# Performance work log

Hardware: AMD Instinct MI355X
Metric: run time of the kernel (lower is better)

The kernel has to match this reference:

```python
import jax, jax.numpy as jnp
import numpy as np

B, T, C, H, N, FF = 2, 1024, 2048, 32, 64, 8192
DIV = 8.0  # head_size_divisor
LAYER_ID, N_LAYER = 1, 24
EPS = 1e-5


def _layer_norm(x, g, b):
    m = x.mean(-1, keepdims=True)
    v = x.var(-1, keepdims=True)
    return (x - m) / jnp.sqrt(v + EPS) * g + b


def _group_norm(x, g, b):
    # GroupNorm(H, C) applied per token: normalize each head's N channels
    xg = x.reshape(B, T, H, N)
    m = xg.mean(-1, keepdims=True)
    v = xg.var(-1, keepdims=True)
    xn = ((xg - m) / jnp.sqrt(v + EPS)).reshape(B, T, C)
    return xn * g + b


def _time_shift(x):
    # xx[t] = x[t-1], xx[0] = 0
    return jnp.pad(x, ((0, 0), (1, 0), (0, 0)))[:, :-1]


def _wkv5(r, k, v, w, u):
    # r,k,v: [B,T,H,N]; w,u: [H,N]. Linear recurrence with per-channel decay.
    decay = jnp.exp(-jnp.exp(w))            # [H,N]
    dec = decay[None, :, :, None]           # broadcast over B and v-dim
    uu = u[None, :, :, None]
    rs = jnp.moveaxis(r, 1, 0)              # [T,B,H,N]
    ks = jnp.moveaxis(k, 1, 0)
    vs = jnp.moveaxis(v, 1, 0)

    def step(state, inp):                   # state: [B,H,N,N] (k-dim i, v-dim j)
        rt, kt, vt = inp
        kv = kt[..., :, None] * vt[..., None, :]          # [B,H,N,N]
        y = jnp.einsum('bhi,bhij->bhj', rt, uu * kv + state)
        return dec * state + kv, y

    state0 = jnp.zeros((B, H, N, N), r.dtype)
    _, ys = jax.lax.scan(step, state0, (rs, ks, vs))
    return jnp.moveaxis(ys, 0, 1).reshape(B, T, C)


def _forward(x, ln1_g, ln1_b, ln2_g, ln2_b,
             tm_k, tm_v, tm_r, tm_g, time_decay, time_faaaa,
             Wr, Wk, Wv, Wg, Wo, lnx_g, lnx_b,
             fm_k, fm_r, Wkey, Wrec, Wval):
    # ---- TimeMix ----
    xl = _layer_norm(x, ln1_g, ln1_b)
    xx = _time_shift(xl)
    xk = xl * tm_k + xx * (1 - tm_k)
    xv = xl * tm_v + xx * (1 - tm_v)
    xr = xl * tm_r + xx * (1 - tm_r)
    xg = xl * tm_g + xx * (1 - tm_g)
    r = (xr @ Wr).reshape(B, T, H, N)
    k = (xk @ Wk).reshape(B, T, H, N)
    v = (xv @ Wv).reshape(B, T, H, N)
    g = jax.nn.silu(xg @ Wg)
    att = _wkv5(r, k, v, time_decay, time_faaaa)
    att = _group_norm(att / DIV, lnx_g, lnx_b)
    x = x + (att * g) @ Wo
    # ---- ChannelMix ----
    xl2 = _layer_norm(x, ln2_g, ln2_b)
    xx2 = _time_shift(xl2)
    ck = xl2 * fm_k + xx2 * (1 - fm_k)
    cr = xl2 * fm_r + xx2 * (1 - fm_r)
    kk = jnp.square(jax.nn.relu(ck @ Wkey))
    kv = kk @ Wval
    return x + jax.nn.sigmoid(cr @ Wrec) * kv


def setup_inputs() -> dict:
    key = jax.random.key(0)
    ks = jax.random.split(key, 9)
    r01 = LAYER_ID / (N_LAYER - 1)
    r1a0 = 1.0 - LAYER_ID / N_LAYER
    ddd = (np.arange(C, dtype=np.float64) / C)[None, None, :]
    dec = np.array([-6 + 5 * (n / (C - 1)) ** (0.7 + 1.3 * r01) for n in range(C)])
    faa = np.array([r01 * (1 - n / (C - 1)) + ((n + 1) % 3 - 1) * 0.1 for n in range(C)])
    f32 = lambda a: jnp.asarray(a, jnp.float32)
    w = lambda k_, i, o: jax.random.normal(k_, (i, o), jnp.float32) * (i ** -0.5)
    return {
        'x': jax.random.normal(ks[0], (B, T, C), jnp.float32),
        'ln1_g': jnp.ones((C,), jnp.float32), 'ln1_b': jnp.zeros((C,), jnp.float32),
        'ln2_g': jnp.ones((C,), jnp.float32), 'ln2_b': jnp.zeros((C,), jnp.float32),
        'tm_k': f32(ddd ** r1a0), 'tm_v': f32(ddd ** r1a0 + 0.3 * r01),
        'tm_r': f32(ddd ** (0.5 * r1a0)), 'tm_g': f32(ddd ** (0.5 * r1a0)),
        'time_decay': f32(dec.reshape(H, N)), 'time_faaaa': f32(faa.reshape(H, N)),
        'Wr': w(ks[1], C, C), 'Wk': w(ks[2], C, C), 'Wv': w(ks[3], C, C),
        'Wg': w(ks[4], C, C), 'Wo': w(ks[5], C, C),
        'lnx_g': jnp.ones((C,), jnp.float32), 'lnx_b': jnp.zeros((C,), jnp.float32),
        'fm_k': f32(ddd ** r1a0), 'fm_r': f32(ddd ** r1a0),
        'Wkey': w(ks[6], C, FF), 'Wrec': w(ks[7], C, C), 'Wval': w(ks[8], FF, C),
    }


def reference(x, ln1_g, ln1_b, ln2_g, ln2_b,
              tm_k, tm_v, tm_r, tm_g, time_decay, time_faaaa,
              Wr, Wk, Wv, Wg, Wo, lnx_g, lnx_b,
              fm_k, fm_r, Wkey, Wrec, Wval):
    return _forward(x, ln1_g, ln1_b, ln2_g, ln2_b,
                    tm_k, tm_v, tm_r, tm_g, time_decay, time_faaaa,
                    Wr, Wk, Wv, Wg, Wo, lnx_g, lnx_b,
                    fm_k, fm_r, Wkey, Wrec, Wval)
```

## Files before the change

kernel.cpp:

```cpp
#include <hip/hip_runtime.h>
#include <stdint.h>

#define BB 2
#define TT 1024
#define CC 2048
#define HH 32
#define NNH 64
#define FFD 8192
#define MTOT (BB*TT)
#define LNEPS 1e-5f
#define LOG2E 1.44269504088896340736f

typedef __attribute__((ext_vector_type(8))) __bf16 bf16x8;
typedef __attribute__((ext_vector_type(4))) float f32x4;

#define USE_GLL 1
typedef __attribute__((address_space(1))) void GAS;
typedef __attribute__((address_space(3))) void LAS;

__device__ inline void gload_lds16(const uint16_t* g, uint16_t* l) {
#if USE_GLL
  __builtin_amdgcn_global_load_lds((GAS*)g, (LAS*)l, 16, 0, 0);
#else
  *(uint4*)l = *(const uint4*)g;
#endif
}

__device__ inline float bf2f(uint32_t u) {
  union { uint32_t i; float f; } v; v.i = u << 16; return v.f;
}
__device__ inline uint16_t f2bf(float f) {
  union { float f; uint32_t i; } v; v.f = f;
  uint32_t r = v.i + 0x7FFFu + ((v.i >> 16) & 1u);
  return (uint16_t)(r >> 16);
}
__device__ inline void unpack8(uint4 d, float* v) {
  v[0] = bf2f(d.x & 0xffffu); v[1] = bf2f(d.x >> 16);
  v[2] = bf2f(d.y & 0xffffu); v[3] = bf2f(d.y >> 16);
  v[4] = bf2f(d.z & 0xffffu); v[5] = bf2f(d.z >> 16);
  v[6] = bf2f(d.w & 0xffffu); v[7] = bf2f(d.w >> 16);
}
__device__ inline uint4 pack8(const float* v) {
  uint4 d;
  d.x = (uint32_t)f2bf(v[0]) | ((uint32_t)f2bf(v[1]) << 16);
  d.y = (uint32_t)f2bf(v[2]) | ((uint32_t)f2bf(v[3]) << 16);
  d.z = (uint32_t)f2bf(v[4]) | ((uint32_t)f2bf(v[5]) << 16);
  d.w = (uint32_t)f2bf(v[6]) | ((uint32_t)f2bf(v[7]) << 16);
  return d;
}

__device__ inline void load8f(const void* p, size_t idx, int fl, float* v) {
  if (fl) {
    const float* q = (const float*)p + idx;
    float4 a = *(const float4*)q; float4 b = *(const float4*)(q + 4);
    v[0]=a.x; v[1]=a.y; v[2]=a.z; v[3]=a.w; v[4]=b.x; v[5]=b.y; v[6]=b.z; v[7]=b.w;
  } else {
    unpack8(*(const uint4*)((const uint16_t*)p + idx), v);
  }
}
__device__ inline float load1f(const void* p, size_t idx, int fl) {
  return fl ? ((const float*)p)[idx] : bf2f(((const uint16_t*)p)[idx]);
}

__global__ void probe_kernel(const uint16_t* __restrict__ x, int* __restrict__ flag) {
  int tid = threadIdx.x;
  float m = 0.f;
  for (int i = tid; i < 4096; i += 64) {
    float a = fabsf(bf2f(x[i]));
    if (a > m) m = a;
  }
  for (int o = 32; o; o >>= 1) { float t = __shfl_down(m, o); if (t > m) m = t; }
  if (tid == 0) *flag = (m > 1e6f) ? 1 : 0;
}

template<int INMODE>
__global__ __launch_bounds__(256) void ln_kernel(const void* __restrict__ x,
    const void* __restrict__ g, const void* __restrict__ b,
    uint16_t* __restrict__ out, const int* __restrict__ dflag)
{
  int fl = *dflag;
  int row = blockIdx.x;
  int tid = threadIdx.x;
  int lane = tid & 63, wave = tid >> 6;
  size_t base = (size_t)row * CC + (size_t)tid * 8;
  float v[8];
  if constexpr (INMODE == 1) {
    const float* q = (const float*)x + base;
    float4 a = *(const float4*)q; float4 c = *(const float4*)(q + 4);
    v[0]=a.x; v[1]=a.y; v[2]=a.z; v[3]=a.w; v[4]=c.x; v[5]=c.y; v[6]=c.z; v[7]=c.w;
  } else {
    load8f(x, base, fl, v);
  }
  float s = 0.f, s2 = 0.f;
  #pragma unroll
  for (int j = 0; j < 8; j++) { s += v[j]; s2 += v[j] * v[j]; }
  for (int o = 32; o; o >>= 1) { s += __shfl_down(s, o); s2 += __shfl_down(s2, o); }
  __shared__ float red[8];
  if (lane == 0) { red[wave] = s; red[wave + 4] = s2; }
  __syncthreads();
  s  = red[0] + red[1] + red[2] + red[3];
  s2 = red[4] + red[5] + red[6] + red[7];
  float mean = s * (1.0f / CC);
  float var  = s2 * (1.0f / CC) - mean * mean;
  float rstd = rsqrtf(fmaxf(var, 0.f) + LNEPS);
  float gj[8], bj[8];
  load8f(g, (size_t)tid * 8, fl, gj);
  load8f(b, (size_t)tid * 8, fl, bj);
  float o8[8];
  #pragma unroll
  for (int j = 0; j < 8; j++) o8[j] = (v[j] - mean) * rstd * gj[j] + bj[j];
  *(uint4*)(out + base) = pack8(o8);
}

__global__ __launch_bounds__(256) void mix4_kernel(const uint16_t* __restrict__ xl,
    const void* __restrict__ tmr, const void* __restrict__ tmk,
    const void* __restrict__ tmv, const void* __restrict__ tmg,
    uint16_t* __restrict__ out, const int* __restrict__ dflag)
{
  int fl = *dflag;
  uint32_t idx = ((uint32_t)blockIdx.x * 256u + threadIdx.x) * 8u;
  uint32_t c = idx & (CC - 1);
  uint32_t row = idx >> 11;
  uint32_t t = row & (TT - 1);
  float xv[8], pv[8];
  unpack8(*(const uint4*)(xl + idx), xv);
  if (t) { unpack8(*(const uint4*)(xl + idx - CC), pv); }
  else   { for (int j = 0; j < 8; j++) pv[j] = 0.f; }
  const void* tms[4] = { tmr, tmk, tmv, tmg };
  const size_t SL = (size_t)MTOT * CC;
  #pragma unroll
  for (int a = 0; a < 4; a++) {
    float tm[8], o[8];
    load8f(tms[a], c, fl, tm);
    #pragma unroll
    for (int j = 0; j < 8; j++) o[j] = xv[j] * tm[j] + pv[j] * (1.f - tm[j]);
    *(uint4*)(out + a * SL + idx) = pack8(o);
  }
}

__global__ __launch_bounds__(256) void mix2_kernel(const uint16_t* __restrict__ xl,
    const void* __restrict__ tk, const void* __restrict__ tr,
    uint16_t* __restrict__ ok, uint16_t* __restrict__ orr,
    const int* __restrict__ dflag)
{
  int fl = *dflag;
  uint32_t idx = ((uint32_t)blockIdx.x * 256u + threadIdx.x) * 8u;
  uint32_t c = idx & (CC - 1);
  uint32_t row = idx >> 11;
  uint32_t t = row & (TT - 1);
  float xv[8], pv[8], tm[8], o[8];
  unpack8(*(const uint4*)(xl + idx), xv);
  if (t) { unpack8(*(const uint4*)(xl + idx - CC), pv); }
  else   { for (int j = 0; j < 8; j++) pv[j] = 0.f; }
  load8f(tk, c, fl, tm);
  #pragma unroll
  for (int j = 0; j < 8; j++) o[j] = xv[j] * tm[j] + pv[j] * (1.f - tm[j]);
  *(uint4*)(ok + idx) = pack8(o);
  load8f(tr, c, fl, tm);
  #pragma unroll
  for (int j = 0; j < 8; j++) o[j] = xv[j] * tm[j] + pv[j] * (1.f - tm[j]);
  *(uint4*)(orr + idx) = pack8(o);
}

__device__ inline void transpose_tile(const void* W, uint16_t* WT, int Kd, int Nd,
                                      int n0, int k0, int fl, int tid)
{
  __shared__ __align__(16) uint16_t tile[64][66];
  int r = tid >> 3, s = tid & 7;
  #pragma unroll
  for (int p = 0; p < 2; p++) {
    int row = p * 32 + r;
    float tv[8];
    load8f(W, (size_t)(k0 + row) * Nd + n0 + s * 8, fl, tv);
    uint16_t* t = &tile[row][s * 8];
    #pragma unroll
    for (int e = 0; e < 8; e++) t[e] = f2bf(tv[e]);
  }
  __syncthreads();
  #pragma unroll
  for (int p = 0; p < 2; p++) {
    int row = p * 32 + r;
    uint16_t tmp[8];
    #pragma unroll
    for (int e = 0; e < 8; e++) tmp[e] = tile[s * 8 + e][row];
    uint4 o;
    o.x = (uint32_t)tmp[0] | ((uint32_t)tmp[1] << 16);
    o.y = (uint32_t)tmp[2] | ((uint32_t)tmp[3] << 16);
    o.z = (uint32_t)tmp[4] | ((uint32_t)tmp[5] << 16);
    o.w = (uint32_t)tmp[6] | ((uint32_t)tmp[7] << 16);
    *(uint4*)(WT + (size_t)(n0 + row) * Kd + k0 + s * 8) = o;
  }
}

__global__ __launch_bounds__(256) void transpose_kernel(const void* __restrict__ W,
    uint16_t* __restrict__ WT, int Kd, int Nd, const int* __restrict__ dflag)
{
  transpose_tile(W, WT, Kd, Nd, blockIdx.x * 64, blockIdx.y * 64, *dflag, threadIdx.x);
}

__global__ __launch_bounds__(256) void transpose4_kernel(
    const void* __restrict__ W0, const void* __restrict__ W1,
    const void* __restrict__ W2, const void* __restrict__ W3,
    uint16_t* __restrict__ WT, const int* __restrict__ dflag)
{
  const void* Ws[4] = { W0, W1, W2, W3 };
  int z = blockIdx.z;
  transpose_tile(Ws[z], WT + (size_t)z * CC * CC, CC, CC,
                 blockIdx.x * 64, blockIdx.y * 64, *dflag, threadIdx.x);
}

enum { EPI_RESID = 2, EPI_SIGM = 9 };

template<int EPI>
__global__ __launch_bounds__(256, 2) void gemm_kernel(
    const uint16_t* __restrict__ Ain, const uint16_t* __restrict__ BTin,
    void* __restrict__ Cout, int N, int Kstride, int Kloop,
    const void* __restrict__ auxA, const int* __restrict__ dflag)
{
  const uint16_t* A  = Ain;
  const uint16_t* BT = BTin;
  uint16_t* co16 = (uint16_t*)Cout;
  float*    co32 = (float*)Cout;
  int fl = 0;
  if constexpr (EPI == EPI_RESID) fl = *dflag;
  int bx = blockIdx.x;
  int N_ = N;
  int n0 = bx * 128;
  int m0 = blockIdx.y * 128;
  __shared__ __align__(16) uint16_t As[128 * 64];
  __shared__ __align__(16) uint16_t Bs[128 * 64];
  int tid = threadIdx.x;
  int lane = tid & 63, wave = tid >> 6;
  int wm = (wave >> 1) * 64, wn = (wave & 1) * 64;
  int l15 = lane & 15, lq = lane >> 4;
  int sw = l15 & 7;
  f32x4 acc[4][4];
  #pragma unroll
  for (int i = 0; i < 4; i++)
    #pragma unroll
    for (int j = 0; j < 4; j++) acc[i][j] = 0.f;
  const int rr = tid >> 3, seg = tid & 7;
  const int sseg = (seg ^ (rr & 7)) * 8;
  const uint16_t* Ag = A + (size_t)(m0 + rr) * Kstride + sseg;
  const uint16_t* Bg = BT + (size_t)(n0 + rr) * Kstride + sseg;
  uint16_t* Asw = As + tid * 8;
  uint16_t* Bsw = Bs + tid * 8;
  for (int k0 = 0; k0 < Kloop; k0 += 64) {
    __syncthreads();
    #pragma unroll
    for (int p = 0; p < 4; p++) {
      gload_lds16(Ag + (size_t)p * 32 * Kstride + k0, Asw + p * 2048);
      gload_lds16(Bg + (size_t)p * 32 * Kstride + k0, Bsw + p * 2048);
    }
    __syncthreads();
    #pragma unroll
    for (int kk = 0; kk < 2; kk++) {
      int cidx = ((kk * 4 + lq) ^ sw) * 8;
      bf16x8 af[4], bv[4];
      #pragma unroll
      for (int f = 0; f < 4; f++) af[f] = *(const bf16x8*)&As[(wm + f * 16 + l15) * 64 + cidx];
      #pragma unroll
      for (int f = 0; f < 4; f++) bv[f] = *(const bf16x8*)&Bs[(wn + f * 16 + l15) * 64 + cidx];
      #pragma unroll
      for (int fm = 0; fm < 4; fm++)
        #pragma unroll
        for (int fn = 0; fn < 4; fn++)
          acc[fm][fn] = __builtin_amdgcn_mfma_f32_16x16x32_bf16(af[fm], bv[fn], acc[fm][fn], 0, 0, 0);
    }
  }
  #pragma unroll
  for (int fm = 0; fm < 4; fm++) {
    #pragma unroll
    for (int q = 0; q < 4; q++) {
      int gr = m0 + wm + fm * 16 + lq * 4 + q;
      size_t rowb = (size_t)gr * N_;
      #pragma unroll
      for (int fn = 0; fn < 4; fn++) {
        int gc = n0 + wn + fn * 16 + l15;
        size_t idx = rowb + gc;
        float val = acc[fm][fn][q];
        if constexpr (EPI == EPI_RESID) {
          co32[idx] = val + load1f(auxA, idx, fl);
        } else if constexpr (EPI == EPI_SIGM) {
          co16[idx] = f2bf(1.f / (1.f + __expf(-val)));
        }
      }
    }
  }
}

enum { G_RKVG = 0, G_KK = 1, G_PART = 2 };

template<int EPI>
__global__ __launch_bounds__(512, 2) void gemm256_kernel(
    const uint16_t* __restrict__ Ain, const uint16_t* __restrict__ BTin,
    void* __restrict__ Cout, int N, int Kstride, int Kloop, int cx,
    float* __restrict__ p2, float* __restrict__ p3a, float* __restrict__ p3b)
{
  __shared__ __align__(16) uint16_t smem[65536];
  const uint16_t* A  = Ain;
  const uint16_t* BT = BTin;
  uint16_t* co16 = (uint16_t*)Cout;
  float*    co32 = (float*)Cout;

  uint32_t lid = ((uint32_t)blockIdx.z * gridDim.y + blockIdx.y) * gridDim.x + blockIdx.x;
  uint32_t xcd = lid & 7u, s = lid >> 3;
  uint32_t lx = s % (uint32_t)cx, ly = s / (uint32_t)cx;
  uint32_t sx = gridDim.x / (uint32_t)cx;
  uint32_t cxi = xcd % sx, cyi = xcd / sx;
  uint32_t gx  = cxi * (uint32_t)cx + lx;
  uint32_t gyz = cyi * (32u / (uint32_t)cx) + ly;
  uint32_t gy  = gyz % gridDim.y;
  uint32_t z   = gyz / gridDim.y;

  int n0 = (int)gx * 256;
  int m0 = (int)gy * 256;
  bool silu = false;
  if constexpr (EPI == G_RKVG) {
    A    += (size_t)z * MTOT * CC;
    BT   += (size_t)z * CC * CC;
    co16 += (size_t)z * MTOT * CC;
    silu = (z == 3);
  }
  if constexpr (EPI == G_PART) {
    A  += (size_t)z * Kloop;
    BT += (size_t)z * Kloop;
    if (z < 2)      co32 += (size_t)z * MTOT * 2048;
    else if (z == 2) co32 = p2;
    else            co32 = (m0 < 1024) ? p3a : (p3b - (size_t)1024 * 2048);
  }
  const int tid  = threadIdx.x;
  const int lane = tid & 63, wave = tid >> 6;
  const int wm = wave >> 2;
  const int wn = wave & 3;
  const int l15 = lane & 15, lq = lane >> 4;
  const int sw = l15 & 7;
  const int c0 = ((0 * 4 + lq) ^ sw) * 8;
  const int c1 = ((1 * 4 + lq) ^ sw) * 8;

  const int trow = tid >> 3;
  const int tswz = ((tid & 7) ^ (trow & 7)) * 8;
  const uint16_t* Ag = A  + ((size_t)m0 + trow) * Kstride + tswz;
  const uint16_t* Bg = BT + ((size_t)n0 + trow) * Kstride + tswz;
  uint16_t* ldsT = smem + tid * 8;
  const size_t r64K = (size_t)64 * Kstride;

  const uint16_t* aRd = smem + (wm * 64 + l15) * 64;
  const uint16_t* bRd = smem + 32768 + (wn * 32 + l15) * 64;

  bf16x8 a[4][2];
  bf16x8 bb[2][2][2];
  f32x4  acc[2][4][2][2];
  #pragma unroll
  for (int mh = 0; mh < 2; mh++)
    #pragma unroll
    for (int f = 0; f < 4; f++)
      #pragma unroll
      for (int nh = 0; nh < 2; nh++)
        #pragma unroll
        for (int g = 0; g < 2; g++) acc[mh][f][nh][g] = 0.f;

#define STG(Mg, matOff, d, h, kt) do { \
    const uint16_t* s_ = (Mg) + (size_t)((h) * 128) * Kstride + (size_t)(kt) * 64; \
    uint16_t* l_ = ldsT + (matOff) + (d) * 16384 + (h) * 8192; \
    gload_lds16(s_, l_); \
    gload_lds16(s_ + r64K, l_ + 4096); \
  } while (0)

#define RD_A(mh, d) do { \
    const uint16_t* p_ = aRd + (d) * 16384 + (mh) * 8192; \
    _Pragma("unroll") \
    for (int f = 0; f < 4; f++) { \
      a[f][0] = *(const bf16x8*)(p_ + f * 1024 + c0); \
      a[f][1] = *(const bf16x8*)(p_ + f * 1024 + c1); \
    } \
  } while (0)

#define RD_B(nh, d) do { \
    const uint16_t* p_ = bRd + (d) * 16384 + (nh) * 8192; \
    _Pragma("unroll") \
    for (int g = 0; g < 2; g++) { \
      bb[nh][g][0] = *(const bf16x8*)(p_ + g * 1024 + c0); \
      bb[nh][g][1] = *(const bf16x8*)(p_ + g * 1024 + c1); \
    } \
  } while (0)

#define QUAD(mh, nh) do { \
    __builtin_amdgcn_s_setprio(1); \
    _Pragma("unroll") \
    for (int f = 0; f < 4; f++) \
      _Pragma("unroll") \
      for (int g = 0; g < 2; g++) { \
        acc[mh][f][nh][g] = __builtin_amdgcn_mfma_f32_16x16x32_bf16(a[f][0], bb[nh][g][0], acc[mh][f][nh][g], 0, 0, 0); \
        acc[mh][f][nh][g] = __builtin_amdgcn_mfma_f32_16x16x32_bf16(a[f][1], bb[nh][g][1], acc[mh][f][nh][g], 0, 0, 0); \
      } \
    __builtin_amdgcn_s_setprio(0); \
  } while (0)

#define TILE(t, d) do { \
     \
    RD_A(0, d); RD_B(0, d); \
    if ((t) + 1 < NT) STG(Ag, 0, (d) ^ 1, 1, (t) + 1); \
    __builtin_amdgcn_s_barrier(); \
    asm volatile("s_waitcnt lgkmcnt(0)" ::: "memory"); \
    QUAD(0, 0); \
    __builtin_amdgcn_s_barrier(); \
     \
    RD_B(1, d); \
    if ((t) + 2 < NT) STG(Ag, 0, d, 0, (t) + 2); \
    __builtin_amdgcn_s_barrier(); \
    asm volatile("s_waitcnt lgkmcnt(0)" ::: "memory"); \
    QUAD(0, 1); \
    __builtin_amdgcn_s_barrier(); \
     \
    RD_A(1, d); \
    if ((t) + 2 < NT) STG(Bg, 32768, d, 0, (t) + 2); \
    __builtin_amdgcn_s_barrier(); \
    asm volatile("s_waitcnt lgkmcnt(0)" ::: "memory"); \
    QUAD(1, 1); \
    __builtin_amdgcn_s_barrier(); \
     \
    if ((t) + 2 < NT) STG(Bg, 32768, d, 1, (t) + 2); \
    __builtin_amdgcn_s_barrier(); \
    QUAD(1, 0); \
    if ((t) + 2 < NT)      { asm volatile("s_waitcnt vmcnt(6)" ::: "memory"); } \
    else if ((t) + 1 < NT) { asm volatile("s_waitcnt vmcnt(0)" ::: "memory"); } \
    __builtin_amdgcn_s_barrier(); \
  } while (0)

  const int NT = Kloop >> 6;
  STG(Ag, 0, 0, 0, 0); STG(Ag, 0, 0, 1, 0);
  STG(Bg, 32768, 0, 0, 0); STG(Bg, 32768, 0, 1, 0);
  if (NT > 1) {
    STG(Ag, 0, 1, 0, 1); STG(Bg, 32768, 1, 0, 1); STG(Bg, 32768, 1, 1, 1);
    asm volatile("s_waitcnt vmcnt(6)" ::: "memory");
  } else {
    asm volatile("s_waitcnt vmcnt(0)" ::: "memory");
  }
  __builtin_amdgcn_s_barrier();

  for (int t = 0; t < NT; t += 2) {
    TILE(t, 0);
    TILE(t + 1, 1);
  }

#undef TILE
#undef QUAD
#undef RD_B
#undef RD_A
#undef STG

  #pragma unroll
  for (int mh = 0; mh < 2; mh++) {
    #pragma unroll
    for (int f = 0; f < 4; f++) {
      #pragma unroll
      for (int q = 0; q < 4; q++) {
        int gr = m0 + mh * 128 + wm * 64 + f * 16 + lq * 4 + q;
        size_t rowb = (size_t)gr * N;
        #pragma unroll
        for (int nh = 0; nh < 2; nh++) {
          #pragma unroll
          for (int g = 0; g < 2; g++) {
            int gc = n0 + nh * 128 + wn * 32 + g * 16 + l15;
            size_t idx = rowb + gc;
            float val = acc[mh][f][nh][g][q];
            if constexpr (EPI == G_RKVG) {
              if (silu) val = val / (1.f + __expf(-fmaxf(val, -80.f)));
              co16[idx] = f2bf(val);
            } else if constexpr (EPI == G_KK) {
              float tv = fmaxf(val, 0.f);
              co16[idx] = f2bf(tv * tv);
            } else if constexpr (EPI == G_PART) {
              co32[idx] = val;
            }
          }
        }
      }
    }
  }
}

__global__ __launch_bounds__(256) void final_reduce_kernel(
    const float* __restrict__ P, const float* __restrict__ x1,
    const uint16_t* __restrict__ sr, void* __restrict__ out,
    const float* __restrict__ P2, const float* __restrict__ P3a,
    const float* __restrict__ P3b, const int* __restrict__ dflag)
{
  int fl = *dflag;
  size_t idx = ((size_t)blockIdx.x * 256 + threadIdx.x) * 8;
  const float* P1 = P + (size_t)MTOT * 2048;
  const float* P3 = (idx < (size_t)1024 * 2048) ? (P3a + idx) : (P3b + idx - (size_t)1024 * 2048);
  float a[8], b[8], c2[8], d3[8], xv[8], s8[8], o[8];
  { float4 t0 = *(const float4*)(P + idx);  float4 t1 = *(const float4*)(P + idx + 4);
    a[0]=t0.x;a[1]=t0.y;a[2]=t0.z;a[3]=t0.w;a[4]=t1.x;a[5]=t1.y;a[6]=t1.z;a[7]=t1.w; }
  { float4 t0 = *(const float4*)(P1 + idx); float4 t1 = *(const float4*)(P1 + idx + 4);
    b[0]=t0.x;b[1]=t0.y;b[2]=t0.z;b[3]=t0.w;b[4]=t1.x;b[5]=t1.y;b[6]=t1.z;b[7]=t1.w; }
  { float4 t0 = *(const float4*)(P2 + idx); float4 t1 = *(const float4*)(P2 + idx + 4);
    c2[0]=t0.x;c2[1]=t0.y;c2[2]=t0.z;c2[3]=t0.w;c2[4]=t1.x;c2[5]=t1.y;c2[6]=t1.z;c2[7]=t1.w; }
  { float4 t0 = *(const float4*)(P3);       float4 t1 = *(const float4*)(P3 + 4);
    d3[0]=t0.x;d3[1]=t0.y;d3[2]=t0.z;d3[3]=t0.w;d3[4]=t1.x;d3[5]=t1.y;d3[6]=t1.z;d3[7]=t1.w; }
  { float4 t0 = *(const float4*)(x1 + idx); float4 t1 = *(const float4*)(x1 + idx + 4);
    xv[0]=t0.x;xv[1]=t0.y;xv[2]=t0.z;xv[3]=t0.w;xv[4]=t1.x;xv[5]=t1.y;xv[6]=t1.z;xv[7]=t1.w; }
  unpack8(*(const uint4*)(sr + idx), s8);
  #pragma unroll
  for (int j = 0; j < 8; j++) o[j] = xv[j] + s8[j] * (a[j] + b[j] + c2[j] + d3[j]);
  if (fl) {
    float* q = (float*)out + idx;
    *(float4*)q = make_float4(o[0], o[1], o[2], o[3]);
    *(float4*)(q + 4) = make_float4(o[4], o[5], o[6], o[7]);
  } else {
    *(uint4*)((uint16_t*)out + idx) = pack8(o);
  }
}

__global__ __launch_bounds__(256) void wkv_p_kernel(
    const uint16_t* __restrict__ kq, const uint16_t* __restrict__ vq,
    const void* __restrict__ wq, float* __restrict__ P,
    const int* __restrict__ dflag)
{
  int fl = *dflag;
  int blk = blockIdx.x;
  int c = blk & 15, h = (blk >> 4) & 31, b = blk >> 9;
  __shared__ __align__(16) float Kt[64][64];
  __shared__ __align__(16) uint16_t Vb[64][64];
  __shared__ __align__(16) float e_s[64];
  int tid = threadIdx.x;
  if (tid < 64) e_s[tid] = fminf(__expf(load1f(wq, h * 64 + tid, fl)), 100.f);
  __syncthreads();
  int rr = tid >> 3, cs = (tid & 7) * 8;
  #pragma unroll
  for (int p = 0; p < 2; p++) {
    int s = p * 32 + rr;
    size_t gbase = ((size_t)(b * TT + c * 64 + s)) * CC + h * 64 + cs;
    float k8[8];
    unpack8(*(const uint4*)(kq + gbase), k8);
    float sp = (float)(s + 1) * LOG2E;
    #pragma unroll
    for (int j = 0; j < 8; j++) Kt[s][cs + j] = k8[j] * exp2f(fminf(sp * e_s[cs + j], 80.f));
    *(uint4*)&Vb[s][cs] = *(const uint4*)(vq + gbase);
  }
  __syncthreads();
  int tx = tid & 15, ty = tid >> 4;
  int i0 = ty * 4, j0 = tx * 4;
  float acc[4][4] = {};
  for (int s = 0; s < 64; s++) {
    float4 a = *(const float4*)&Kt[s][i0];
    ushort4 vv = *(const ushort4*)&Vb[s][j0];
    float b0 = bf2f(vv.x), b1 = bf2f(vv.y), b2 = bf2f(vv.z), b3 = bf2f(vv.w);
    float am[4] = { a.x, a.y, a.z, a.w };
    #pragma unroll
    for (int m = 0; m < 4; m++) {
      acc[m][0] += am[m] * b0; acc[m][1] += am[m] * b1;
      acc[m][2] += am[m] * b2; acc[m][3] += am[m] * b3;
    }
  }
  float* Pb = P + (size_t)blk * 4096;
  #pragma unroll
  for (int m = 0; m < 4; m++) {
    float dl = exp2f(-64.0f * LOG2E * e_s[i0 + m]);
    float4 o = { acc[m][0] * dl, acc[m][1] * dl, acc[m][2] * dl, acc[m][3] * dl };
    *(float4*)&Pb[(i0 + m) * 64 + j0] = o;
  }
}

__global__ __launch_bounds__(256) void wkv_s_kernel(const float* __restrict__ P,
    const void* __restrict__ wq, float* __restrict__ S,
    const int* __restrict__ dflag)
{
  int fl = *dflag;
  int bh = blockIdx.x;
  int h = bh & 31;
  int tid = threadIdx.x;
  int i = tid >> 2, q = tid & 3;
  float e = fminf(__expf(load1f(wq, h * 64 + i, fl)), 100.f);
  float dl = exp2f(-64.0f * LOG2E * e);
  float4 s0 = {0,0,0,0}, s1 = {0,0,0,0}, s2 = {0,0,0,0}, s3 = {0,0,0,0};
  for (int c = 0; c < 16; c++) {
    size_t base = ((size_t)bh * 16 + c) * 4096 + (size_t)i * 64 + q * 16;
    *(float4*)&S[base + 0]  = s0;
    *(float4*)&S[base + 4]  = s1;
    *(float4*)&S[base + 8]  = s2;
    *(float4*)&S[base + 12] = s3;
    float4 p0 = *(const float4*)&P[base + 0];
    float4 p1 = *(const float4*)&P[base + 4];
    float4 p2 = *(const float4*)&P[base + 8];
    float4 p3 = *(const float4*)&P[base + 12];
    s0 = make_float4(dl * s0.x + p0.x, dl * s0.y + p0.y, dl * s0.z + p0.z, dl * s0.w + p0.w);
    s1 = make_float4(dl * s1.x + p1.x, dl * s1.y + p1.y, dl * s1.z + p1.z, dl * s1.w + p1.w);
    s2 = make_float4(dl * s2.x + p2.x, dl * s2.y + p2.y, dl * s2.z + p2.z, dl * s2.w + p2.w);
    s3 = make_float4(dl * s3.x + p3.x, dl * s3.y + p3.y, dl * s3.z + p3.z, dl * s3.w + p3.w);
  }
}

__global__ __launch_bounds__(256, 2) void wkv_y_kernel(
    const uint16_t* __restrict__ rq, const uint16_t* __restrict__ kq,
    const uint16_t* __restrict__ vq, const void* __restrict__ wq,
    const void* __restrict__ uq, const float* __restrict__ S,
    float* __restrict__ att, const int* __restrict__ dflag)
{
  int fl = *dflag;
  int blk = blockIdx.x;
  int c = blk & 15, h = (blk >> 4) & 31, b = blk >> 9;
  __shared__ __align__(16) float Rt[64][64];
  __shared__ __align__(16) float Kt[64][64];
  __shared__ __align__(16) uint16_t Vb[64][64];
  __shared__ __align__(16) float Ss[64][64];
  __shared__ __align__(16) float e_s[64];
  __shared__ __align__(16) float ud_s[64];
  int tid = threadIdx.x;
  if (tid < 64) {
    float e = fminf(__expf(load1f(wq, h * 64 + tid, fl)), 100.f);
    e_s[tid] = e;
    ud_s[tid] = load1f(uq, h * 64 + tid, fl) * __expf(-e);
  }
  __syncthreads();
  int rr = tid >> 3, cs = (tid & 7) * 8;
  #pragma unroll
  for (int p = 0; p < 2; p++) {
    int s = p * 32 + rr;
    size_t gbase = ((size_t)(b * TT + c * 64 + s)) * CC + h * 64 + cs;
    float r8[8], k8[8];
    unpack8(*(const uint4*)(rq + gbase), r8);
    unpack8(*(const uint4*)(kq + gbase), k8);
    float tneg = -(float)s * LOG2E;
    float spos = (float)(s + 1) * LOG2E;
    #pragma unroll
    for (int j = 0; j < 8; j++) {
      float e = e_s[cs + j];
      Rt[s][cs + j] = r8[j] * exp2f(tneg * e);
      Kt[s][cs + j] = k8[j] * exp2f(fminf(spos * e, 80.f));
    }
    *(uint4*)&Vb[s][cs] = *(const uint4*)(vq + gbase);
  }
  {
    int r2 = tid >> 2, q = tid & 3;
    const float* Sbp = S + (size_t)blk * 4096 + (size_t)r2 * 64 + q * 16;
    *(float4*)&Ss[r2][q * 16 + 0]  = *(const float4*)&Sbp[0];
    *(float4*)&Ss[r2][q * 16 + 4]  = *(const float4*)&Sbp[4];
    *(float4*)&Ss[r2][q * 16 + 8]  = *(const float4*)&Sbp[8];
    *(float4*)&Ss[r2][q * 16 + 12] = *(const float4*)&Sbp[12];
  }
  __syncthreads();
  int tx = tid & 15, ty = tid >> 4;
  int t0 = ty * 4, s0 = tx * 4;
  float acc[4][4] = {};
  for (int iq = 0; iq < 16; iq++) {
    int i = iq * 4;
    float4 ra[4], kb[4];
    #pragma unroll
    for (int m = 0; m < 4; m++) ra[m] = *(const float4*)&Rt[t0 + m][i];
    #pragma unroll
    for (int n = 0; n < 4; n++) kb[n] = *(const float4*)&Kt[s0 + n][i];
    #pragma unroll
    for (int m = 0; m < 4; m++)
      #pragma unroll
      for (int n = 0; n < 4; n++)
        acc[m][n] += ra[m].x * kb[n].x + ra[m].y * kb[n].y + ra[m].z * kb[n].z + ra[m].w * kb[n].w;
  }
  float dg = 0.f;
  if (tid < 64) {
    for (int iq = 0; iq < 16; iq++) {
      int i = iq * 4;
      float4 a = *(const float4*)&Rt[tid][i];
      float4 kk = *(const float4*)&Kt[tid][i];
      float4 u4 = *(const float4*)&ud_s[i];
      dg += a.x * kk.x * u4.x + a.y * kk.y * u4.y + a.z * kk.z * u4.z + a.w * kk.w * u4.w;
    }
  }
  __syncthreads();
  #pragma unroll
  for (int m = 0; m < 4; m++)
    #pragma unroll
    for (int n = 0; n < 4; n++) {
      int t = t0 + m, s = s0 + n;
      Kt[t][s] = (s < t) ? acc[m][n] : 0.0f;
    }
  __syncthreads();
  if (tid < 64) Kt[tid][tid] = dg;
  __syncthreads();
  int j0 = tx * 4;
  float y[4][4] = {};
  for (int sq = 0; sq < 16; sq++) {
    int s = sq * 4;
    float4 a4[4];
    #pragma unroll
    for (int m = 0; m < 4; m++) a4[m] = *(const float4*)&Kt[t0 + m][s];
    float vb[4][4];
    #pragma unroll
    for (int qq = 0; qq < 4; qq++) {
      ushort4 vv = *(const ushort4*)&Vb[s + qq][j0];
      vb[qq][0] = bf2f(vv.x); vb[qq][1] = bf2f(vv.y); vb[qq][2] = bf2f(vv.z); vb[qq][3] = bf2f(vv.w);
    }
    #pragma unroll
    for (int m = 0; m < 4; m++)
      #pragma unroll
      for (int n = 0; n < 4; n++)
        y[m][n] += a4[m].x * vb[0][n] + a4[m].y * vb[1][n] + a4[m].z * vb[2][n] + a4[m].w * vb[3][n];
  }
  for (int iq = 0; iq < 16; iq++) {
    int i = iq * 4;
    float4 r4[4], s4[4];
    #pragma unroll
    for (int m = 0; m < 4; m++) r4[m] = *(const float4*)&Rt[t0 + m][i];
    #pragma unroll
    for (int qq = 0; qq < 4; qq++) s4[qq] = *(const float4*)&Ss[i + qq][j0];
    #pragma unroll
    for (int m = 0; m < 4; m++)
      #pragma unroll
      for (int n = 0; n < 4; n++)
        y[m][n] += r4[m].x * s4[0][n] + r4[m].y * s4[1][n] + r4[m].z * s4[2][n] + r4[m].w * s4[3][n];
  }
  #pragma unroll
  for (int m = 0; m < 4; m++) {
    size_t ob = ((size_t)(b * TT + c * 64 + t0 + m)) * CC + h * 64 + j0;
    *(float4*)&att[ob] = make_float4(y[m][0], y[m][1], y[m][2], y[m][3]);
  }
}

__global__ __launch_bounds__(256) void gn_mul_kernel(const float* __restrict__ att,
    const void* __restrict__ gg, const void* __restrict__ bb,
    const uint16_t* __restrict__ gate, uint16_t* __restrict__ out,
    const int* __restrict__ dflag)
{
  int fl = *dflag;
  int row = blockIdx.x;
  int tid = threadIdx.x;
  size_t base = (size_t)row * CC + (size_t)tid * 8;
  float4 a0 = *(const float4*)(att + base);
  float4 a1 = *(const float4*)(att + base + 4);
  float v[8] = { a0.x, a0.y, a0.z, a0.w, a1.x, a1.y, a1.z, a1.w };
  #pragma unroll
  for (int j = 0; j < 8; j++) v[j] *= 0.125f;
  float s = 0.f, s2 = 0.f;
  #pragma unroll
  for (int j = 0; j < 8; j++) { s += v[j]; s2 += v[j] * v[j]; }
  s += __shfl_xor(s, 1); s += __shfl_xor(s, 2); s += __shfl_xor(s, 4);
  s2 += __shfl_xor(s2, 1); s2 += __shfl_xor(s2, 2); s2 += __shfl_xor(s2, 4);
  float m = s * (1.f / 64.f);
  float var = s2 * (1.f / 64.f) - m * m;
  float rstd = rsqrtf(fmaxf(var, 0.f) + LNEPS);
  int c = tid * 8;
  float g8[8], b8[8], gt8[8], o[8];
  load8f(gg, c, fl, g8);
  load8f(bb, c, fl, b8);
  unpack8(*(const uint4*)(gate + base), gt8);
  #pragma unroll
  for (int j = 0; j < 8; j++) o[j] = ((v[j] - m) * rstd * g8[j] + b8[j]) * gt8[j];
  *(uint4*)(out + base) = pack8(o);
}

extern "C" void kernel_launch(void* const* d_in, const int* in_sizes, int n_in,
                              void* d_out, int out_size, void* d_ws, size_t ws_size,
                              hipStream_t stream)
{
  const void* x    = d_in[0];
  const void* ln1g = d_in[1];
  const void* ln1b = d_in[2];
  const void* ln2g = d_in[3];
  const void* ln2b = d_in[4];
  const void* tmk  = d_in[5];
  const void* tmv  = d_in[6];
  const void* tmr  = d_in[7];
  const void* tmg  = d_in[8];
  const void* tdec = d_in[9];
  const void* tfaa = d_in[10];
  const void* Wr   = d_in[11];
  const void* Wk   = d_in[12];
  const void* Wv   = d_in[13];
  const void* Wg   = d_in[14];
  const void* Wo   = d_in[15];
  const void* lnxg = d_in[16];
  const void* lnxb = d_in[17];
  const void* fmk  = d_in[18];
  const void* fmr  = d_in[19];
  const void* Wkey = d_in[20];
  const void* Wrec = d_in[21];
  const void* Wval = d_in[22];

  char* ws = (char*)d_ws;
  const size_t SL  = (size_t)MTOT * CC;
  uint16_t* XL    = (uint16_t*)(ws + 0);
  uint16_t* WRECT = XL;
  uint16_t* MIX4  = (uint16_t*)(ws + 8388608);
  float*    PART  = (float*)   (ws + 8388608);
  uint16_t* RKVG  = (uint16_t*)(ws + 41943040);
  float*    ATT   = (float*)   (ws + 75497472);
  float*    X1    = ATT;
  float*    Pb    = (float*)   (ws + 92274688);
  float*    Sb    = (float*)   (ws + 109051904);
  uint16_t* KK    = (uint16_t*)(ws + 92274688);
  uint16_t* WT    = (uint16_t*)(ws + 125829120);
  int*      FLAG  = (int*)     (ws + 159383552);
  (void)in_sizes; (void)n_in; (void)out_size; (void)ws_size;

  probe_kernel<<<dim3(1), 64, 0, stream>>>((const uint16_t*)x, FLAG);
  ln_kernel<0><<<dim3(MTOT), 256, 0, stream>>>(x, ln1g, ln1b, XL, FLAG);
  transpose4_kernel<<<dim3(32, 32, 4), 256, 0, stream>>>(Wr, Wk, Wv, Wg, WT, FLAG);
  mix4_kernel<<<dim3(2048), 256, 0, stream>>>(XL, tmr, tmk, tmv, tmg, MIX4, FLAG);
  gemm256_kernel<G_RKVG><<<dim3(8, 8, 4), 512, 0, stream>>>(MIX4, WT, (void*)RKVG, CC, CC, CC, 8,
      nullptr, nullptr, nullptr);
  wkv_p_kernel<<<dim3(1024), 256, 0, stream>>>(RKVG + 1 * SL, RKVG + 2 * SL, tdec, Pb, FLAG);
  wkv_s_kernel<<<dim3(64), 256, 0, stream>>>(Pb, tdec, Sb, FLAG);
  wkv_y_kernel<<<dim3(1024), 256, 0, stream>>>(RKVG + 0 * SL, RKVG + 1 * SL, RKVG + 2 * SL, tdec, tfaa, Sb, ATT, FLAG);
  gn_mul_kernel<<<dim3(MTOT), 256, 0, stream>>>(ATT, lnxg, lnxb, RKVG + 3 * SL, MIX4, FLAG);
  transpose_kernel<<<dim3(32, 32), 256, 0, stream>>>(Wo, WT, CC, CC, FLAG);
  gemm_kernel<EPI_RESID><<<dim3(16, 16), 256, 0, stream>>>(MIX4, WT, (void*)X1, CC, CC, CC,
      x, FLAG);
  ln_kernel<1><<<dim3(MTOT), 256, 0, stream>>>(X1, ln2g, ln2b, XL, FLAG);
  mix2_kernel<<<dim3(2048), 256, 0, stream>>>(XL, fmk, fmr, MIX4, RKVG, FLAG);
  transpose_kernel<<<dim3(FFD / 64, CC / 64), 256, 0, stream>>>(Wkey, WT, CC, FFD, FLAG);
  transpose_kernel<<<dim3(32, 32), 256, 0, stream>>>(Wrec, WRECT, CC, CC, FLAG);
  gemm256_kernel<G_KK><<<dim3(32, 8), 512, 0, stream>>>(MIX4, WT, (void*)KK, FFD, CC, CC, 4,
      nullptr, nullptr, nullptr);
  gemm_kernel<EPI_SIGM><<<dim3(16, 16), 256, 0, stream>>>(RKVG, WRECT, (void*)(RKVG + 2 * SL), CC, CC, CC,
      nullptr, FLAG);
  transpose_kernel<<<dim3(CC / 64, FFD / 64), 256, 0, stream>>>(Wval, WT, FFD, CC, FLAG);
  gemm256_kernel<G_PART><<<dim3(8, 8, 4), 512, 0, stream>>>(KK, WT, (void*)PART, CC, FFD, FFD / 4, 8,
      (float*)RKVG, (float*)XL, (float*)(RKVG + 3 * SL));
  final_reduce_kernel<<<dim3(2048), 256, 0, stream>>>(PART, X1, RKVG + 2 * SL, d_out,
      (float*)RKVG, (float*)XL, (float*)(RKVG + 3 * SL), FLAG);
}
```

Measured before the change: 719.3 us.

## Software-pipeline LDS fragment reads across GEMM quadrants with double-buffered registers

The GEMM main loop now prefetches the next tile's A0/B0 fragments from LDS during the last quadrant of the current tile and ping-pongs two B0 register sets. Several s_barrier plus lgkmcnt waits before each MFMA quadrant become sched_barriers, so LDS reads overlap with MFMA work instead of stalling. This raises register pressure by holding extra fragment buffers, and it relies on the compiler to insert the needed lgkmcnt waits after the explicit waits were removed.

```diff
diff --git a/kernel.cpp b/kernel.cpp
--- a/kernel.cpp
+++ b/kernel.cpp
@@ -348,8 +348,8 @@
   const uint16_t* aRd = smem + (wm * 64 + l15) * 64;
   const uint16_t* bRd = smem + 32768 + (wn * 32 + l15) * 64;
 
-  bf16x8 a[4][2];
-  bf16x8 bb[2][2][2];
+  bf16x8 a0_[4][2], a1_[4][2];
+  bf16x8 b1_[2][2], b0a_[2][2], b0b_[2][2];
   f32x4  acc[2][4][2][2];
   #pragma unroll
   for (int mh = 0; mh < 2; mh++)
@@ -367,64 +367,62 @@
     gload_lds16(s_ + r64K, l_ + 4096); \
   } while (0)
 
-#define RD_A(mh, d) do { \
+#define RDA(dst, d, mh) do { \
     const uint16_t* p_ = aRd + (d) * 16384 + (mh) * 8192; \
     _Pragma("unroll") \
     for (int f = 0; f < 4; f++) { \
-      a[f][0] = *(const bf16x8*)(p_ + f * 1024 + c0); \
-      a[f][1] = *(const bf16x8*)(p_ + f * 1024 + c1); \
+      dst[f][0] = *(const bf16x8*)(p_ + f * 1024 + c0); \
+      dst[f][1] = *(const bf16x8*)(p_ + f * 1024 + c1); \
     } \
   } while (0)
 
-#define RD_B(nh, d) do { \
+#define RDB(dst, d, nh) do { \
     const uint16_t* p_ = bRd + (d) * 16384 + (nh) * 8192; \
     _Pragma("unroll") \
     for (int g = 0; g < 2; g++) { \
-      bb[nh][g][0] = *(const bf16x8*)(p_ + g * 1024 + c0); \
-      bb[nh][g][1] = *(const bf16x8*)(p_ + g * 1024 + c1); \
+      dst[g][0] = *(const bf16x8*)(p_ + g * 1024 + c0); \
+      dst[g][1] = *(const bf16x8*)(p_ + g * 1024 + c1); \
     } \
   } while (0)
 
-#define QUAD(mh, nh) do { \
+#define QUAD(AR, BR, mh, nh) do { \
     __builtin_amdgcn_s_setprio(1); \
     _Pragma("unroll") \
     for (int f = 0; f < 4; f++) \
       _Pragma("unroll") \
       for (int g = 0; g < 2; g++) { \
-        acc[mh][f][nh][g] = __builtin_amdgcn_mfma_f32_16x16x32_bf16(a[f][0], bb[nh][g][0], acc[mh][f][nh][g], 0, 0, 0); \
-        acc[mh][f][nh][g] = __builtin_amdgcn_mfma_f32_16x16x32_bf16(a[f][1], bb[nh][g][1], acc[mh][f][nh][g], 0, 0, 0); \
+        acc[mh][f][nh][g] = __builtin_amdgcn_mfma_f32_16x16x32_bf16(AR[f][0], BR[g][0], acc[mh][f][nh][g], 0, 0, 0); \
+        acc[mh][f][nh][g] = __builtin_amdgcn_mfma_f32_16x16x32_bf16(AR[f][1], BR[g][1], acc[mh][f][nh][g], 0, 0, 0); \
       } \
     __builtin_amdgcn_s_setprio(0); \
   } while (0)
 
-#define TILE(t, d) do { \
+#define TILE(t, d, B0C, B0N) do { \
      \
-    RD_A(0, d); RD_B(0, d); \
+    RDB(b1_, d, 1); \
     if ((t) + 1 < NT) STG(Ag, 0, (d) ^ 1, 1, (t) + 1); \
-    __builtin_amdgcn_s_barrier(); \
-    asm volatile("s_waitcnt lgkmcnt(0)" ::: "memory"); \
-    QUAD(0, 0); \
+    __builtin_amdgcn_sched_barrier(0); \
+    QUAD(a0_, B0C, 0, 0); \
     __builtin_amdgcn_s_barrier(); \
      \
-    RD_B(1, d); \
+    RDA(a1_, d, 1); \
     if ((t) + 2 < NT) STG(Ag, 0, d, 0, (t) + 2); \
-    __builtin_amdgcn_s_barrier(); \
-    asm volatile("s_waitcnt lgkmcnt(0)" ::: "memory"); \
-    QUAD(0, 1); \
+    __builtin_amdgcn_sched_barrier(0); \
+    QUAD(a0_, b1_, 0, 1); \
     __builtin_amdgcn_s_barrier(); \
      \
-    RD_A(1, d); \
     if ((t) + 2 < NT) STG(Bg, 32768, d, 0, (t) + 2); \
-    __builtin_amdgcn_s_barrier(); \
-    asm volatile("s_waitcnt lgkmcnt(0)" ::: "memory"); \
-    QUAD(1, 1); \
+    __builtin_amdgcn_sched_barrier(0); \
+    QUAD(a1_, b1_, 1, 1); \
     __builtin_amdgcn_s_barrier(); \
      \
     if ((t) + 2 < NT) STG(Bg, 32768, d, 1, (t) + 2); \
-    __builtin_amdgcn_s_barrier(); \
-    QUAD(1, 0); \
     if ((t) + 2 < NT)      { asm volatile("s_waitcnt vmcnt(6)" ::: "memory"); } \
     else if ((t) + 1 < NT) { asm volatile("s_waitcnt vmcnt(0)" ::: "memory"); } \
+    __builtin_amdgcn_s_barrier();    \
+    if ((t) + 1 < NT) { RDA(a0_, (d) ^ 1, 0); RDB(B0N, (d) ^ 1, 0); } \
+    __builtin_amdgcn_sched_barrier(0); \
+    QUAD(a1_, B0C, 1, 0); \
     __builtin_amdgcn_s_barrier(); \
   } while (0)
 
@@ -438,16 +436,17 @@
     asm volatile("s_waitcnt vmcnt(0)" ::: "memory");
   }
   __builtin_amdgcn_s_barrier();
+  RDA(a0_, 0, 0); RDB(b0a_, 0, 0);
 
   for (int t = 0; t < NT; t += 2) {
-    TILE(t, 0);
-    TILE(t + 1, 1);
+    TILE(t, 0, b0a_, b0b_);
+    TILE(t + 1, 1, b0b_, b0a_);
   }
 
 #undef TILE
 #undef QUAD
-#undef RD_B
-#undef RD_A
+#undef RDB
+#undef RDA
 #undef STG
 
   #pragma unroll
```

Result: slower. 1.236 ms (+71.8%).
